# Performance work log

Hardware: AMD Instinct MI355X
Metric: run time of the kernel (lower is better)

The kernel has to match this reference:

```python
import jax, jax.numpy as jnp
import numpy as np
from jax import lax

T, IN, H, B = 256, 2048, 2048, 8
K_INIT = 4.0

def setup_inputs() -> dict:
    key = jax.random.key(0)
    k1, k2, k3, k4, k5, k6 = jax.random.split(key, 6)
    k = 1.0 / np.sqrt(H)
    # simplex-init alphas: off-diagonal -K, diagonal log(1-(B-1)exp(-K)), plus small noise
    base = jnp.full((B, B), -K_INIT) + jnp.eye(B) * (np.log(1.0 - (B - 1) * np.exp(-K_INIT)) + K_INIT)
    alphas = base + 0.01 * jax.random.normal(k1, (B, B))
    return {
        "x": jax.random.normal(k2, (T, IN), dtype=jnp.float32),            # sentence of word vectors
        "W": jax.random.uniform(k3, (B, H, H), minval=-k, maxval=k),       # B recurrent basis matrices
        "alphas": alphas.astype(jnp.float32),                               # [B, B] mixing logits
        "bias": jax.random.uniform(k4, (H,), minval=-k, maxval=k),
        "v": jnp.eye(H, IN, dtype=jnp.float32),                             # input projection (init = eye)
        "fc_w": jax.random.uniform(k5, (H, H), minval=-k, maxval=k),
        "fc_b": jax.random.uniform(k6, (H,), minval=-k, maxval=k),
        "alpha_int": 0,
    }

def reference(x, W, alphas, bias, v, fc_w, fc_b, alpha_int):
    # normalise_alpha == softmax over the selected alpha row (simplex=True)
    alpha = jax.nn.softmax(alphas[alpha_int])                 # [B]
    u = jnp.einsum('b,bij->ij', alpha, W)                     # mixed recurrent weight [H, H]
    igates = x @ v.T                                          # all input gates at once [T, H]

    def step(h, ig):                                          # Elman cell: h = tanh(v@w + u@h + bias)
        h = jnp.tanh(ig + u @ h + bias)
        return h, None

    h0 = jnp.zeros((H,), dtype=x.dtype)
    h, _ = lax.scan(step, h0, igates)                         # sequential over T words
    out = jax.nn.sigmoid(h @ fc_w.T + fc_b)                   # fc(hidden.t()) then sigmoid
    return out[None, :]                                       # [1, H]
```

## Files before the change

### kernel.cpp

```cpp
#include <hip/hip_runtime.h>
#include <math.h>

#define HDIM    2048
#define TSTEPS  256
#define BBASIS  8
#define RING_D  4
#define NR      8

typedef float f32x4 __attribute__((ext_vector_type(4)));

__device__ inline void store_coherent_f4(float* p, f32x4 v) {
    asm volatile("global_store_dwordx4 %0, %1, off sc0 sc1"
                 :: "v"(p), "v"(v) : "memory");
}
__device__ inline f32x4 load_coherent_f4(const float* p) {
    f32x4 a;
    asm volatile("global_load_dwordx4 %0, %1, off sc0 sc1\n\t"
                 "s_waitcnt vmcnt(0)"
                 : "=&v"(a) : "v"(p) : "memory");
    return a;
}

__global__ __launch_bounds__(256, 1)
void prep_kernel(const float* __restrict__ x,
                 const float* __restrict__ W,
                 const float* __restrict__ alphas,
                 const float* __restrict__ v,
                 const int*   __restrict__ alpha_int,
                 float*       __restrict__ u_g,
                 float*       __restrict__ ig_g)
{
    const int tid  = threadIdx.x;
    const int bid  = blockIdx.x;
    const int wave = tid >> 6;
    const int lane = tid & 63;
    const int r0   = bid * 8 + wave * 2;

    __shared__ __align__(16) float x_tile[8][HDIM];

    const int ai = alpha_int[0];
    float a[BBASIS];
    float mx = -1e30f;
    #pragma unroll
    for (int b = 0; b < BBASIS; ++b) { a[b] = alphas[ai * BBASIS + b]; mx = fmaxf(mx, a[b]); }
    float ssum = 0.f;
    #pragma unroll
    for (int b = 0; b < BBASIS; ++b) { a[b] = expf(a[b] - mx); ssum += a[b]; }
    const float inv_s = 1.f / ssum;

    {
        float acc[2][8][4];
        #pragma unroll
        for (int q = 0; q < 2; ++q)
            #pragma unroll
            for (int k = 0; k < 8; ++k)
                #pragma unroll
                for (int i = 0; i < 4; ++i) acc[q][k][i] = 0.f;

        for (int b = 0; b < BBASIS; ++b) {
            const float ab = a[b] * inv_s;
            #pragma unroll
            for (int q = 0; q < 2; ++q) {
                const f32x4* wrow = (const f32x4*)(W + ((size_t)b * HDIM + (size_t)(r0 + q)) * HDIM);
                #pragma unroll
                for (int k = 0; k < 8; ++k) {
                    f32x4 w4 = wrow[lane + 64 * k];
                    acc[q][k][0] += ab * w4.x;
                    acc[q][k][1] += ab * w4.y;
                    acc[q][k][2] += ab * w4.z;
                    acc[q][k][3] += ab * w4.w;
                }
            }
        }
        #pragma unroll
        for (int q = 0; q < 2; ++q) {
            f32x4* urow = (f32x4*)(u_g + (size_t)(r0 + q) * HDIM);
            #pragma unroll
            for (int k = 0; k < 8; ++k) {
                f32x4 w4;
                w4.x = acc[q][k][0]; w4.y = acc[q][k][1];
                w4.z = acc[q][k][2]; w4.w = acc[q][k][3];
                urow[lane + 64 * k] = w4;
            }
        }
    }

    {
        float vr[2][8][4];
        #pragma unroll
        for (int q = 0; q < 2; ++q) {
            const f32x4* vrow = (const f32x4*)(v + (size_t)(r0 + q) * HDIM);
            #pragma unroll
            for (int k = 0; k < 8; ++k) {
                f32x4 t4 = vrow[lane + 64 * k];
                vr[q][k][0] = t4.x; vr[q][k][1] = t4.y; vr[q][k][2] = t4.z; vr[q][k][3] = t4.w;
            }
        }
        for (int tb = 0; tb < TSTEPS; tb += 8) {
            #pragma unroll
            for (int j = 0; j < 8; ++j) {
                const f32x4* xt4 = (const f32x4*)(x + (size_t)(tb + j) * HDIM);
                #pragma unroll
                for (int c = 0; c < 2; ++c)
                    ((f32x4*)x_tile[j])[tid + 256 * c] = xt4[tid + 256 * c];
            }
            __syncthreads();
            #pragma unroll
            for (int j = 0; j < 8; ++j) {
                float acc0 = 0.f, acc1 = 0.f;
                #pragma unroll
                for (int k = 0; k < 8; ++k) {
                    const f32x4 x4 = ((const f32x4*)x_tile[j])[lane + 64 * k];
                    acc0 += vr[0][k][0]*x4.x + vr[0][k][1]*x4.y + vr[0][k][2]*x4.z + vr[0][k][3]*x4.w;
                    acc1 += vr[1][k][0]*x4.x + vr[1][k][1]*x4.y + vr[1][k][2]*x4.z + vr[1][k][3]*x4.w;
                }
                #pragma unroll
                for (int off = 32; off > 0; off >>= 1) {
                    acc0 += __shfl_xor(acc0, off, 64);
                    acc1 += __shfl_xor(acc1, off, 64);
                }
                if (lane == 0)
                    *(float2*)&ig_g[(size_t)(tb + j) * HDIM + r0] = make_float2(acc0, acc1);
            }
            __syncthreads();
        }
    }
}

__global__ __launch_bounds__(512, 1)
void scan_kernel(const float* __restrict__ bias,
                 const float* __restrict__ fc_w,
                 const float* __restrict__ fc_b,
                 float*       __restrict__ out,
                 const float* __restrict__ u_g,
                 const float* __restrict__ ig_g,
                 float*       __restrict__ ring)
{
    const int tid  = threadIdx.x;
    const int bid  = blockIdx.x;
    const int wave = tid >> 6;
    const int lane = tid & 63;
    const int r0   = bid * 32 + wave * 4;

    __shared__ __align__(16) float h_lds[2][HDIM];
    __shared__ __align__(16) float ig_lds[TSTEPS][32];

    #pragma unroll
    for (int i = 0; i < 4; ++i) {
        const int c  = tid + 512 * i;
        const int t  = c >> 3;
        const int ch = c & 7;
        f32x4 g = *(const f32x4*)&ig_g[(size_t)t * HDIM + bid * 32 + ch * 4];
        *(f32x4*)&ig_lds[t][ch * 4] = g;
    }

    float u_reg[4][8][4];
    #pragma unroll
    for (int q = 0; q < 4; ++q) {
        const f32x4* urow = (const f32x4*)(u_g + (size_t)(r0 + q) * HDIM);
        #pragma unroll
        for (int k = 0; k < 8; ++k) {
            f32x4 w4 = urow[lane + 64 * k];
            u_reg[q][k][0] = w4.x; u_reg[q][k][1] = w4.y;
            u_reg[q][k][2] = w4.z; u_reg[q][k][3] = w4.w;
        }
    }
    float bias4[4];
    #pragma unroll
    for (int q = 0; q < 4; ++q) bias4[q] = bias[r0 + q];

    h_lds[0][tid]        = 0.f;
    h_lds[0][tid + 512]  = 0.f;
    h_lds[0][tid + 1024] = 0.f;
    h_lds[0][tid + 1536] = 0.f;
    __syncthreads();

    int cur = 0;
    for (int t = 0; t < TSTEPS; ++t) {
        float acc0 = 0.f, acc1 = 0.f, acc2 = 0.f, acc3 = 0.f;
        #pragma unroll
        for (int k = 0; k < 8; ++k) {
            const f32x4 h4 = ((const f32x4*)h_lds[cur])[lane + 64 * k];
            acc0 += u_reg[0][k][0]*h4.x + u_reg[0][k][1]*h4.y + u_reg[0][k][2]*h4.z + u_reg[0][k][3]*h4.w;
            acc1 += u_reg[1][k][0]*h4.x + u_reg[1][k][1]*h4.y + u_reg[1][k][2]*h4.z + u_reg[1][k][3]*h4.w;
            acc2 += u_reg[2][k][0]*h4.x + u_reg[2][k][1]*h4.y + u_reg[2][k][2]*h4.z + u_reg[2][k][3]*h4.w;
            acc3 += u_reg[3][k][0]*h4.x + u_reg[3][k][1]*h4.y + u_reg[3][k][2]*h4.z + u_reg[3][k][3]*h4.w;
        }
        #pragma unroll
        for (int off = 32; off > 0; off >>= 1) {
            acc0 += __shfl_xor(acc0, off, 64);
            acc1 += __shfl_xor(acc1, off, 64);
            acc2 += __shfl_xor(acc2, off, 64);
            acc3 += __shfl_xor(acc3, off, 64);
        }
        const int   st     = t + 1;
        const float bias_f = ((st >> 2) & 1) ? 8.0f : -8.0f;
        float* slotbase = ring + (size_t)((st & (RING_D - 1)) * NR) * HDIM;

        const f32x4 ig4 = *(const f32x4*)&ig_lds[t][wave * 4];
        f32x4 hv;
        hv.x = tanhf(acc0 + ig4.x + bias4[0]) + bias_f;
        hv.y = tanhf(acc1 + ig4.y + bias4[1]) + bias_f;
        hv.z = tanhf(acc2 + ig4.z + bias4[2]) + bias_f;
        hv.w = tanhf(acc3 + ig4.w + bias4[3]) + bias_f;
        if (lane < NR)
            store_coherent_f4(slotbase + (size_t)lane * HDIM + r0, hv);

        const float* pp = slotbase + (size_t)(bid & (NR - 1)) * HDIM + 4 * tid;
        f32x4 hq = load_coherent_f4(pp);
        if (bias_f > 0.0f) {
            while (!((hq.x > 6.5f) & (hq.y > 6.5f) & (hq.z > 6.5f) & (hq.w > 6.5f))) {
                __builtin_amdgcn_s_sleep(1);
                hq = load_coherent_f4(pp);
            }
        } else {
            while (!((hq.x < -6.5f) & (hq.y < -6.5f) & (hq.z < -6.5f) & (hq.w < -6.5f))) {
                __builtin_amdgcn_s_sleep(1);
                hq = load_coherent_f4(pp);
            }
        }
        hq.x -= bias_f; hq.y -= bias_f; hq.z -= bias_f; hq.w -= bias_f;

        const int nxt = cur ^ 1;
        *(f32x4*)&h_lds[nxt][4 * tid] = hq;
        __syncthreads();
        cur = nxt;
    }

    {
        float acc0 = 0.f, acc1 = 0.f, acc2 = 0.f, acc3 = 0.f;
        const f32x4* f0 = (const f32x4*)(fc_w + (size_t)(r0 + 0) * HDIM);
        const f32x4* f1 = (const f32x4*)(fc_w + (size_t)(r0 + 1) * HDIM);
        const f32x4* f2 = (const f32x4*)(fc_w + (size_t)(r0 + 2) * HDIM);
        const f32x4* f3 = (const f32x4*)(fc_w + (size_t)(r0 + 3) * HDIM);
        #pragma unroll
        for (int k = 0; k < 8; ++k) {
            const f32x4 h4 = ((const f32x4*)h_lds[cur])[lane + 64 * k];
            f32x4 w0 = f0[lane + 64 * k];
            f32x4 w1 = f1[lane + 64 * k];
            f32x4 w2 = f2[lane + 64 * k];
            f32x4 w3 = f3[lane + 64 * k];
            acc0 += w0.x*h4.x + w0.y*h4.y + w0.z*h4.z + w0.w*h4.w;
            acc1 += w1.x*h4.x + w1.y*h4.y + w1.z*h4.z + w1.w*h4.w;
            acc2 += w2.x*h4.x + w2.y*h4.y + w2.z*h4.z + w2.w*h4.w;
            acc3 += w3.x*h4.x + w3.y*h4.y + w3.z*h4.z + w3.w*h4.w;
        }
        #pragma unroll
        for (int off = 32; off > 0; off >>= 1) {
            acc0 += __shfl_xor(acc0, off, 64);
            acc1 += __shfl_xor(acc1, off, 64);
            acc2 += __shfl_xor(acc2, off, 64);
            acc3 += __shfl_xor(acc3, off, 64);
        }
        if (lane == 0) {
            f32x4 o4;
            o4.x = 1.f / (1.f + expf(-(acc0 + fc_b[r0 + 0])));
            o4.y = 1.f / (1.f + expf(-(acc1 + fc_b[r0 + 1])));
            o4.z = 1.f / (1.f + expf(-(acc2 + fc_b[r0 + 2])));
            o4.w = 1.f / (1.f + expf(-(acc3 + fc_b[r0 + 3])));
            *(f32x4*)&out[r0] = o4;
        }
    }
}

__global__ __launch_bounds__(512, 1)
void elman_scan_self(const float* __restrict__ x,
                     const float* __restrict__ W,
                     const float* __restrict__ alphas,
                     const float* __restrict__ bias,
                     const float* __restrict__ v,
                     const float* __restrict__ fc_w,
                     const float* __restrict__ fc_b,
                     const int*   __restrict__ alpha_int,
                     float*       __restrict__ out,
                     float*       __restrict__ hbuf)
{
    const int tid  = threadIdx.x;
    const int bid  = blockIdx.x;
    const int wave = tid >> 6;
    const int lane = tid & 63;
    const int r0   = bid * 32 + wave * 4;

    __shared__ __align__(16) float x_tile[8][HDIM];
    __shared__ __align__(16) float ig_lds[TSTEPS][32];
    __shared__ __align__(16) float h_lds[2][HDIM];

    const int ai = alpha_int[0];
    float a[BBASIS];
    float mx = -1e30f;
    #pragma unroll
    for (int b = 0; b < BBASIS; ++b) { a[b] = alphas[ai * BBASIS + b]; mx = fmaxf(mx, a[b]); }
    float ssum = 0.f;
    #pragma unroll
    for (int b = 0; b < BBASIS; ++b) { a[b] = expf(a[b] - mx); ssum += a[b]; }
    const float inv_s = 1.f / ssum;

    {
        float vr[4][8][4];
        #pragma unroll
        for (int q = 0; q < 4; ++q) {
            const f32x4* vrow = (const f32x4*)(v + (size_t)(r0 + q) * HDIM);
            #pragma unroll
            for (int k = 0; k < 8; ++k) {
                f32x4 t4 = vrow[lane + 64 * k];
                vr[q][k][0] = t4.x; vr[q][k][1] = t4.y; vr[q][k][2] = t4.z; vr[q][k][3] = t4.w;
            }
        }
        for (int tb = 0; tb < TSTEPS; tb += 8) {
            #pragma unroll
            for (int j = 0; j < 8; ++j)
                *(f32x4*)&x_tile[j][4 * tid] =
                    *(const f32x4*)&x[(size_t)(tb + j) * HDIM + 4 * tid];
            __syncthreads();
            #pragma unroll
            for (int j = 0; j < 8; ++j) {
                float acc0 = 0.f, acc1 = 0.f, acc2 = 0.f, acc3 = 0.f;
                #pragma unroll
                for (int k = 0; k < 8; ++k) {
                    const f32x4 x4 = ((const f32x4*)x_tile[j])[lane + 64 * k];
                    acc0 += vr[0][k][0]*x4.x + vr[0][k][1]*x4.y + vr[0][k][2]*x4.z + vr[0][k][3]*x4.w;
                    acc1 += vr[1][k][0]*x4.x + vr[1][k][1]*x4.y + vr[1][k][2]*x4.z + vr[1][k][3]*x4.w;
                    acc2 += vr[2][k][0]*x4.x + vr[2][k][1]*x4.y + vr[2][k][2]*x4.z + vr[2][k][3]*x4.w;
                    acc3 += vr[3][k][0]*x4.x + vr[3][k][1]*x4.y + vr[3][k][2]*x4.z + vr[3][k][3]*x4.w;
                }
                #pragma unroll
                for (int off = 32; off > 0; off >>= 1) {
                    acc0 += __shfl_xor(acc0, off, 64);
                    acc1 += __shfl_xor(acc1, off, 64);
                    acc2 += __shfl_xor(acc2, off, 64);
                    acc3 += __shfl_xor(acc3, off, 64);
                }
                if (lane == 0) {
                    f32x4 ig4; ig4.x = acc0; ig4.y = acc1; ig4.z = acc2; ig4.w = acc3;
                    *(f32x4*)&ig_lds[tb + j][wave * 4] = ig4;
                }
            }
            __syncthreads();
        }
    }

    float u_reg[4][8][4];
    #pragma unroll
    for (int q = 0; q < 4; ++q)
        #pragma unroll
        for (int k = 0; k < 8; ++k)
            #pragma unroll
            for (int i = 0; i < 4; ++i) u_reg[q][k][i] = 0.f;

    for (int b = 0; b < BBASIS; ++b) {
        const float ab = a[b] * inv_s;
        #pragma unroll
        for (int q = 0; q < 4; ++q) {
            const f32x4* wrow = (const f32x4*)(W + ((size_t)b * HDIM + (size_t)(r0 + q)) * HDIM);
            #pragma unroll
            for (int k = 0; k < 8; ++k) {
                f32x4 w4 = wrow[lane + 64 * k];
                u_reg[q][k][0] += ab * w4.x;
                u_reg[q][k][1] += ab * w4.y;
                u_reg[q][k][2] += ab * w4.z;
                u_reg[q][k][3] += ab * w4.w;
            }
        }
    }
    float bias4[4];
    #pragma unroll
    for (int q = 0; q < 4; ++q) bias4[q] = bias[r0 + q];

    h_lds[0][tid] = 0.f; h_lds[0][tid + 512] = 0.f;
    h_lds[0][tid + 1024] = 0.f; h_lds[0][tid + 1536] = 0.f;
    __syncthreads();

    int cur = 0;
    for (int t = 0; t < TSTEPS; ++t) {
        float acc0 = 0.f, acc1 = 0.f, acc2 = 0.f, acc3 = 0.f;
        #pragma unroll
        for (int k = 0; k < 8; ++k) {
            const f32x4 h4 = ((const f32x4*)h_lds[cur])[lane + 64 * k];
            acc0 += u_reg[0][k][0]*h4.x + u_reg[0][k][1]*h4.y + u_reg[0][k][2]*h4.z + u_reg[0][k][3]*h4.w;
            acc1 += u_reg[1][k][0]*h4.x + u_reg[1][k][1]*h4.y + u_reg[1][k][2]*h4.z + u_reg[1][k][3]*h4.w;
            acc2 += u_reg[2][k][0]*h4.x + u_reg[2][k][1]*h4.y + u_reg[2][k][2]*h4.z + u_reg[2][k][3]*h4.w;
            acc3 += u_reg[3][k][0]*h4.x + u_reg[3][k][1]*h4.y + u_reg[3][k][2]*h4.z + u_reg[3][k][3]*h4.w;
        }
        #pragma unroll
        for (int off = 32; off > 0; off >>= 1) {
            acc0 += __shfl_xor(acc0, off, 64);
            acc1 += __shfl_xor(acc1, off, 64);
            acc2 += __shfl_xor(acc2, off, 64);
            acc3 += __shfl_xor(acc3, off, 64);
        }
        float* hg = hbuf + (size_t)(t + 1) * HDIM;
        if (lane == 0) {
            const f32x4 ig4 = *(const f32x4*)&ig_lds[t][wave * 4];
            f32x4 hv;
            hv.x = tanhf(acc0 + ig4.x + bias4[0]);
            hv.y = tanhf(acc1 + ig4.y + bias4[1]);
            hv.z = tanhf(acc2 + ig4.z + bias4[2]);
            hv.w = tanhf(acc3 + ig4.w + bias4[3]);
            store_coherent_f4(hg + r0, hv);
        }
        const float* pp = hg + 4 * tid;
        f32x4 hq = load_coherent_f4(pp);
        const unsigned s = 0xFFFFFFFFu;
        while ((__float_as_uint(hq.x) == s) | (__float_as_uint(hq.y) == s) |
               (__float_as_uint(hq.z) == s) | (__float_as_uint(hq.w) == s)) {
            __builtin_amdgcn_s_sleep(1);
            hq = load_coherent_f4(pp);
        }
        const int nxt = cur ^ 1;
        *(f32x4*)&h_lds[nxt][4 * tid] = hq;
        __syncthreads();
        cur = nxt;
    }

    {
        float acc0 = 0.f, acc1 = 0.f, acc2 = 0.f, acc3 = 0.f;
        const f32x4* f0 = (const f32x4*)(fc_w + (size_t)(r0 + 0) * HDIM);
        const f32x4* f1 = (const f32x4*)(fc_w + (size_t)(r0 + 1) * HDIM);
        const f32x4* f2 = (const f32x4*)(fc_w + (size_t)(r0 + 2) * HDIM);
        const f32x4* f3 = (const f32x4*)(fc_w + (size_t)(r0 + 3) * HDIM);
        #pragma unroll
        for (int k = 0; k < 8; ++k) {
            const f32x4 h4 = ((const f32x4*)h_lds[cur])[lane + 64 * k];
            f32x4 w0 = f0[lane + 64 * k];
            f32x4 w1 = f1[lane + 64 * k];
            f32x4 w2 = f2[lane + 64 * k];
            f32x4 w3 = f3[lane + 64 * k];
            acc0 += w0.x*h4.x + w0.y*h4.y + w0.z*h4.z + w0.w*h4.w;
            acc1 += w1.x*h4.x + w1.y*h4.y + w1.z*h4.z + w1.w*h4.w;
            acc2 += w2.x*h4.x + w2.y*h4.y + w2.z*h4.z + w2.w*h4.w;
            acc3 += w3.x*h4.x + w3.y*h4.y + w3.z*h4.z + w3.w*h4.w;
        }
        #pragma unroll
        for (int off = 32; off > 0; off >>= 1) {
            acc0 += __shfl_xor(acc0, off, 64);
            acc1 += __shfl_xor(acc1, off, 64);
            acc2 += __shfl_xor(acc2, off, 64);
            acc3 += __shfl_xor(acc3, off, 64);
        }
        if (lane == 0) {
            f32x4 o4;
            o4.x = 1.f / (1.f + expf(-(acc0 + fc_b[r0 + 0])));
            o4.y = 1.f / (1.f + expf(-(acc1 + fc_b[r0 + 1])));
            o4.z = 1.f / (1.f + expf(-(acc2 + fc_b[r0 + 2])));
            o4.w = 1.f / (1.f + expf(-(acc3 + fc_b[r0 + 3])));
            *(f32x4*)&out[r0] = o4;
        }
    }
}

extern "C" void kernel_launch(void* const* d_in, const int* in_sizes, int n_in,
                              void* d_out, int out_size, void* d_ws, size_t ws_size,
                              hipStream_t stream)
{
    const float* x      = (const float*)d_in[0];
    const float* W      = (const float*)d_in[1];
    const float* alphas = (const float*)d_in[2];
    const float* bias   = (const float*)d_in[3];
    const float* v      = (const float*)d_in[4];
    const float* fc_w   = (const float*)d_in[5];
    const float* fc_b   = (const float*)d_in[6];
    const int*   ai     = (const int*)d_in[7];
    float* out = (float*)d_out;

    const size_t RING_BYTES = (size_t)RING_D * NR * HDIM * sizeof(float);
    const size_t IG_OFF     = 0x80000;
    const size_t U_OFF      = IG_OFF + 0x200000;
    const size_t U_BYTES    = (size_t)HDIM * HDIM * sizeof(float);
    const size_t NEED       = U_OFF + U_BYTES;

    if (ws_size >= NEED) {
        float* ring = (float*)d_ws;
        float* ig_g = (float*)((char*)d_ws + IG_OFF);
        float* u_g  = (float*)((char*)d_ws + U_OFF);
        hipMemsetAsync(d_ws, 0, RING_BYTES, stream);
        prep_kernel<<<256, 256, 0, stream>>>(x, W, alphas, v, ai, u_g, ig_g);
        scan_kernel<<<64, 512, 0, stream>>>(bias, fc_w, fc_b, out, u_g, ig_g, (float*)ring);
    } else {
        float* hbuf = (float*)d_ws;
        const size_t hbuf_bytes = (size_t)(TSTEPS + 1) * HDIM * sizeof(float);
        hipMemsetAsync(d_ws, 0xFF, hbuf_bytes, stream);
        elman_scan_self<<<64, 512, 0, stream>>>(x, W, alphas, bias, v, fc_w, fc_b,
                                                ai, out, hbuf);
    }
}
```

Measured before the change: 995.5 us.

## Poll ring directly per wave and consume chunks as they arrive, drop LDS barrier

Each wave now polls the entire hidden-state vector straight from the coherent ring buffer, eight dwordx4 loads at a time. It accumulates the matvec contribution of each chunk as soon as that chunk's band flag is valid, replacing the per-thread poll, LDS exchange and __syncthreads each step. This removes the block-wide barrier and the LDS round trip from the serial critical path, and overlaps compute with late-arriving chunks. The cost is eight times more coherent global polling traffic per block, since every wave reads the full vector, and a reliance on the sentinel-band encoding for correctness.

```diff
diff --git a/kernel.cpp b/kernel.cpp
--- a/kernel.cpp
+++ b/kernel.cpp
@@ -19,6 +19,28 @@
                  "s_waitcnt vmcnt(0)"
                  : "=&v"(a) : "v"(p) : "memory");
     return a;
+}
+__device__ inline void load8_coherent(const float* p0, const float* p1,
+                                      const float* p2, const float* p3,
+                                      const float* p4, const float* p5,
+                                      const float* p6, const float* p7,
+                                      f32x4& c0, f32x4& c1, f32x4& c2, f32x4& c3,
+                                      f32x4& c4, f32x4& c5, f32x4& c6, f32x4& c7) {
+    asm volatile(
+        "global_load_dwordx4 %0, %8, off sc0 sc1\n\t"
+        "global_load_dwordx4 %1, %9, off sc0 sc1\n\t"
+        "global_load_dwordx4 %2, %10, off sc0 sc1\n\t"
+        "global_load_dwordx4 %3, %11, off sc0 sc1\n\t"
+        "global_load_dwordx4 %4, %12, off sc0 sc1\n\t"
+        "global_load_dwordx4 %5, %13, off sc0 sc1\n\t"
+        "global_load_dwordx4 %6, %14, off sc0 sc1\n\t"
+        "global_load_dwordx4 %7, %15, off sc0 sc1\n\t"
+        "s_waitcnt vmcnt(0)"
+        : "=&v"(c0), "=&v"(c1), "=&v"(c2), "=&v"(c3),
+          "=&v"(c4), "=&v"(c5), "=&v"(c6), "=&v"(c7)
+        : "v"(p0), "v"(p1), "v"(p2), "v"(p3),
+          "v"(p4), "v"(p5), "v"(p6), "v"(p7)
+        : "memory");
 }
 
 __global__ __launch_bounds__(256, 1)
@@ -142,7 +164,6 @@
     const int lane = tid & 63;
     const int r0   = bid * 32 + wave * 4;
 
-    __shared__ __align__(16) float h_lds[2][HDIM];
     __shared__ __align__(16) float ig_lds[TSTEPS][32];
 
     #pragma unroll
@@ -169,23 +190,63 @@
     #pragma unroll
     for (int q = 0; q < 4; ++q) bias4[q] = bias[r0 + q];
 
-    h_lds[0][tid]        = 0.f;
-    h_lds[0][tid + 512]  = 0.f;
-    h_lds[0][tid + 1024] = 0.f;
-    h_lds[0][tid + 1536] = 0.f;
     __syncthreads();
 
-    int cur = 0;
-    for (int t = 0; t < TSTEPS; ++t) {
+    const size_t poll_off  = (size_t)wave * HDIM + 4 * lane;
+    const size_t store_off = r0;
+
+    {
+        const f32x4 ig4 = *(const f32x4*)&ig_lds[0][wave * 4];
+        const float bf = -8.0f;
+        f32x4 hv;
+        hv.x = tanhf(ig4.x + bias4[0]) + bf;
+        hv.y = tanhf(ig4.y + bias4[1]) + bf;
+        hv.z = tanhf(ig4.z + bias4[2]) + bf;
+        hv.w = tanhf(ig4.w + bias4[3]) + bf;
+        float* slotb = ring + (size_t)((1 & (RING_D - 1)) * NR) * HDIM;
+        if (lane < NR)
+            store_coherent_f4(slotb + (size_t)lane * HDIM + store_off, hv);
+    }
+
+    for (int t = 1; t < TSTEPS; ++t) {
+        const int   slot   = t & (RING_D - 1);
+        const bool  bpos   = ((t >> 2) & 1) != 0;
+        const float band_t = bpos ? 8.0f : -8.0f;
+        const float* pp    = ring + (size_t)(slot * NR) * HDIM + poll_off;
+
         float acc0 = 0.f, acc1 = 0.f, acc2 = 0.f, acc3 = 0.f;
-        #pragma unroll
-        for (int k = 0; k < 8; ++k) {
-            const f32x4 h4 = ((const f32x4*)h_lds[cur])[lane + 64 * k];
-            acc0 += u_reg[0][k][0]*h4.x + u_reg[0][k][1]*h4.y + u_reg[0][k][2]*h4.z + u_reg[0][k][3]*h4.w;
-            acc1 += u_reg[1][k][0]*h4.x + u_reg[1][k][1]*h4.y + u_reg[1][k][2]*h4.z + u_reg[1][k][3]*h4.w;
-            acc2 += u_reg[2][k][0]*h4.x + u_reg[2][k][1]*h4.y + u_reg[2][k][2]*h4.z + u_reg[2][k][3]*h4.w;
-            acc3 += u_reg[3][k][0]*h4.x + u_reg[3][k][1]*h4.y + u_reg[3][k][2]*h4.z + u_reg[3][k][3]*h4.w;
-        }
+        unsigned done_mask = 0u;
+        for (;;) {
+            f32x4 c0, c1, c2, c3, c4, c5, c6, c7;
+            load8_coherent(pp,        pp + 256,  pp + 512,  pp + 768,
+                           pp + 1024, pp + 1280, pp + 1536, pp + 1792,
+                           c0, c1, c2, c3, c4, c5, c6, c7);
+            #define CHK(J, CJ)                                                        \
+            if (!(done_mask & (1u << J))) {                                           \
+                bool ok = bpos ? ((CJ.x >  6.5f) & (CJ.y >  6.5f) &                   \
+                                  (CJ.z >  6.5f) & (CJ.w >  6.5f))                    \
+                               : ((CJ.x < -6.5f) & (CJ.y < -6.5f) &                   \
+                                  (CJ.z < -6.5f) & (CJ.w < -6.5f));                   \
+                if (ok) {                                                             \
+                    done_mask |= (1u << J);                                           \
+                    const float hx = CJ.x - band_t, hy = CJ.y - band_t;               \
+                    const float hz = CJ.z - band_t, hw = CJ.w - band_t;               \
+                    acc0 += u_reg[0][J][0]*hx + u_reg[0][J][1]*hy                     \
+                          + u_reg[0][J][2]*hz + u_reg[0][J][3]*hw;                    \
+                    acc1 += u_reg[1][J][0]*hx + u_reg[1][J][1]*hy                     \
+                          + u_reg[1][J][2]*hz + u_reg[1][J][3]*hw;                    \
+                    acc2 += u_reg[2][J][0]*hx + u_reg[2][J][1]*hy                     \
+                          + u_reg[2][J][2]*hz + u_reg[2][J][3]*hw;                    \
+                    acc3 += u_reg[3][J][0]*hx + u_reg[3][J][1]*hy                     \
+                          + u_reg[3][J][2]*hz + u_reg[3][J][3]*hw;                    \
+                } }
+            CHK(0, c0) CHK(1, c1) CHK(2, c2) CHK(3, c3)
+            CHK(4, c4) CHK(5, c5) CHK(6, c6) CHK(7, c7)
+            #undef CHK
+            if (done_mask == 0xFFu) break;
+            __builtin_amdgcn_s_sleep(1);
+        }
+
         #pragma unroll
         for (int off = 32; off > 0; off >>= 1) {
             acc0 += __shfl_xor(acc0, off, 64);
@@ -193,58 +254,60 @@
             acc2 += __shfl_xor(acc2, off, 64);
             acc3 += __shfl_xor(acc3, off, 64);
         }
-        const int   st     = t + 1;
-        const float bias_f = ((st >> 2) & 1) ? 8.0f : -8.0f;
-        float* slotbase = ring + (size_t)((st & (RING_D - 1)) * NR) * HDIM;
-
+
+        const int   st   = t + 1;
+        const float bf   = ((st >> 2) & 1) ? 8.0f : -8.0f;
+        float* slotb = ring + (size_t)((st & (RING_D - 1)) * NR) * HDIM;
         const f32x4 ig4 = *(const f32x4*)&ig_lds[t][wave * 4];
         f32x4 hv;
-        hv.x = tanhf(acc0 + ig4.x + bias4[0]) + bias_f;
-        hv.y = tanhf(acc1 + ig4.y + bias4[1]) + bias_f;
-        hv.z = tanhf(acc2 + ig4.z + bias4[2]) + bias_f;
-        hv.w = tanhf(acc3 + ig4.w + bias4[3]) + bias_f;
+        hv.x = tanhf(acc0 + ig4.x + bias4[0]) + bf;
+        hv.y = tanhf(acc1 + ig4.y + bias4[1]) + bf;
+        hv.z = tanhf(acc2 + ig4.z + bias4[2]) + bf;
+        hv.w = tanhf(acc3 + ig4.w + bias4[3]) + bf;
         if (lane < NR)
-            store_coherent_f4(slotbase + (size_t)lane * HDIM + r0, hv);
-
-        const float* pp = slotbase + (size_t)(bid & (NR - 1)) * HDIM + 4 * tid;
-        f32x4 hq = load_coherent_f4(pp);
-        if (bias_f > 0.0f) {
-            while (!((hq.x > 6.5f) & (hq.y > 6.5f) & (hq.z > 6.5f) & (hq.w > 6.5f))) {
-                __builtin_amdgcn_s_sleep(1);
-                hq = load_coherent_f4(pp);
-            }
-        } else {
-            while (!((hq.x < -6.5f) & (hq.y < -6.5f) & (hq.z < -6.5f) & (hq.w < -6.5f))) {
-                __builtin_amdgcn_s_sleep(1);
-                hq = load_coherent_f4(pp);
-            }
-        }
-        hq.x -= bias_f; hq.y -= bias_f; hq.z -= bias_f; hq.w -= bias_f;
-
-        const int nxt = cur ^ 1;
-        *(f32x4*)&h_lds[nxt][4 * tid] = hq;
-        __syncthreads();
-        cur = nxt;
+            store_coherent_f4(slotb + (size_t)lane * HDIM + store_off, hv);
+    }
+
+    f32x4 h0, h1, h2, h3, h4, h5, h6, h7;
+    {
+        const float* pp = ring + (size_t)(0 * NR) * HDIM + poll_off;
+        unsigned done_mask = 0u;
+        for (;;) {
+            f32x4 c0, c1, c2, c3, c4, c5, c6, c7;
+            load8_coherent(pp,        pp + 256,  pp + 512,  pp + 768,
+                           pp + 1024, pp + 1280, pp + 1536, pp + 1792,
+                           c0, c1, c2, c3, c4, c5, c6, c7);
+            #define GCHK(J, CJ, HJ)                                                   \
+            if (!(done_mask & (1u << J))) {                                           \
+                bool ok = (CJ.x < -6.5f) & (CJ.y < -6.5f) &                           \
+                          (CJ.z < -6.5f) & (CJ.w < -6.5f);                            \
+                if (ok) { done_mask |= (1u << J);                                     \
+                    HJ.x = CJ.x + 8.0f; HJ.y = CJ.y + 8.0f;                           \
+                    HJ.z = CJ.z + 8.0f; HJ.w = CJ.w + 8.0f; } }
+            GCHK(0, c0, h0) GCHK(1, c1, h1) GCHK(2, c2, h2) GCHK(3, c3, h3)
+            GCHK(4, c4, h4) GCHK(5, c5, h5) GCHK(6, c6, h6) GCHK(7, c7, h7)
+            #undef GCHK
+            if (done_mask == 0xFFu) break;
+            __builtin_amdgcn_s_sleep(1);
+        }
     }
 
     {
         float acc0 = 0.f, acc1 = 0.f, acc2 = 0.f, acc3 = 0.f;
-        const f32x4* f0 = (const f32x4*)(fc_w + (size_t)(r0 + 0) * HDIM);
-        const f32x4* f1 = (const f32x4*)(fc_w + (size_t)(r0 + 1) * HDIM);
-        const f32x4* f2 = (const f32x4*)(fc_w + (size_t)(r0 + 2) * HDIM);
-        const f32x4* f3 = (const f32x4*)(fc_w + (size_t)(r0 + 3) * HDIM);
-        #pragma unroll
-        for (int k = 0; k < 8; ++k) {
-            const f32x4 h4 = ((const f32x4*)h_lds[cur])[lane + 64 * k];
-            f32x4 w0 = f0[lane + 64 * k];
-            f32x4 w1 = f1[lane + 64 * k];
-            f32x4 w2 = f2[lane + 64 * k];
-            f32x4 w3 = f3[lane + 64 * k];
-            acc0 += w0.x*h4.x + w0.y*h4.y + w0.z*h4.z + w0.w*h4.w;
-            acc1 += w1.x*h4.x + w1.y*h4.y + w1.z*h4.z + w1.w*h4.w;
-            acc2 += w2.x*h4.x + w2.y*h4.y + w2.z*h4.z + w2.w*h4.w;
-            acc3 += w3.x*h4.x + w3.y*h4.y + w3.z*h4.z + w3.w*h4.w;
-        }
+        #define FCJ(J, HJ)                                                            \
+        {                                                                             \
+            const f32x4 w0 = ((const f32x4*)(fc_w + (size_t)(r0 + 0) * HDIM))[lane + 64 * J]; \
+            const f32x4 w1 = ((const f32x4*)(fc_w + (size_t)(r0 + 1) * HDIM))[lane + 64 * J]; \
+            const f32x4 w2 = ((const f32x4*)(fc_w + (size_t)(r0 + 2) * HDIM))[lane + 64 * J]; \
+            const f32x4 w3 = ((const f32x4*)(fc_w + (size_t)(r0 + 3) * HDIM))[lane + 64 * J]; \
+            acc0 += w0.x*HJ.x + w0.y*HJ.y + w0.z*HJ.z + w0.w*HJ.w;                    \
+            acc1 += w1.x*HJ.x + w1.y*HJ.y + w1.z*HJ.z + w1.w*HJ.w;                    \
+            acc2 += w2.x*HJ.x + w2.y*HJ.y + w2.z*HJ.z + w2.w*HJ.w;                    \
+            acc3 += w3.x*HJ.x + w3.y*HJ.y + w3.z*HJ.z + w3.w*HJ.w;                    \
+        }
+        FCJ(0, h0) FCJ(1, h1) FCJ(2, h2) FCJ(3, h3)
+        FCJ(4, h4) FCJ(5, h5) FCJ(6, h6) FCJ(7, h7)
+        #undef FCJ
         #pragma unroll
         for (int off = 32; off > 0; off >>= 1) {
             acc0 += __shfl_xor(acc0, off, 64);
@@ -474,7 +537,7 @@
         float* u_g  = (float*)((char*)d_ws + U_OFF);
         hipMemsetAsync(d_ws, 0, RING_BYTES, stream);
         prep_kernel<<<256, 256, 0, stream>>>(x, W, alphas, v, ai, u_g, ig_g);
-        scan_kernel<<<64, 512, 0, stream>>>(bias, fc_w, fc_b, out, u_g, ig_g, (float*)ring);
+        scan_kernel<<<64, 512, 0, stream>>>(bias, fc_w, fc_b, out, u_g, ig_g, ring);
     } else {
         float* hbuf = (float*)d_ws;
         const size_t hbuf_bytes = (size_t)(TSTEPS + 1) * HDIM * sizeof(float);
```

After: 1.666 ms. 1.67x slower.
